# Kernel tuning notes

Hardware: AMD Instinct MI355X
Metric: run time of the kernel (lower is better)

The kernel has to match this reference:

```python
import jax, jax.numpy as jnp
import numpy as np

B, A, D, K = 262144, 10, 10, 32  # batch, aspects, aspect dim (=10), projection dim


def setup_inputs() -> dict:
    key = jax.random.key(0)
    ks = jax.random.split(key, 7)
    scale = 0.01
    return {
        "user_rep": jax.random.normal(ks[0], (B, A, D), jnp.float32),
        "item_rep": jax.random.normal(ks[1], (B, A, D), jnp.float32),
        "affinity_matrix": jax.random.uniform(ks[2], (D, D), jnp.float32, -scale, scale),
        "user_projection": jax.random.uniform(ks[3], (K, D), jnp.float32, -scale, scale),
        "user_parameters": jax.random.uniform(ks[4], (K, 1), jnp.float32, -scale, scale),
        "item_projection": jax.random.uniform(ks[5], (K, D), jnp.float32, -scale, scale),
        "item_parameters": jax.random.uniform(ks[6], (K, 1), jnp.float32, -scale, scale),
    }


def reference(user_rep, item_rep, affinity_matrix, user_projection,
              user_parameters, item_projection, item_parameters):
    # affinity: relu( U @ M @ V^T )  -> [B, Au, Av]
    aff = jax.nn.relu(jnp.einsum('bud,de,bve->buv', user_rep, affinity_matrix, item_rep))

    h_user = jnp.einsum('kd,bud->bku', user_projection, user_rep)  # [B,K,Au]
    h_item = jnp.einsum('kd,bvd->bkv', item_projection, item_rep)  # [B,K,Av]

    # user importance branch
    hu = jax.nn.relu(h_user + jnp.einsum('bkv,buv->bku', h_item, aff))
    u_score = jnp.einsum('k,bku->bu', user_parameters[:, 0], hu)   # [B,Au]
    user_asp_importance = jax.nn.softmax(u_score, axis=1)

    # item importance branch
    hi = jax.nn.relu(h_item + jnp.einsum('bku,buv->bkv', h_user, aff))
    i_score = jnp.einsum('k,bkv->bv', item_parameters[:, 0], hi)   # [B,Av]
    item_asp_importance = jax.nn.softmax(i_score, axis=1)

    return (user_asp_importance, item_asp_importance)
```

## Files before the change

### kernel.cpp

```cpp
#include <hip/hip_runtime.h>
#include <hip/hip_bf16.h>

#define NB 262144
#define AA 10
#define DD 10
#define KK 32

static __device__ __forceinline__ float b2f(unsigned short h) {
    union { unsigned u; float f; } c; c.u = ((unsigned)h) << 16; return c.f;
}
static __device__ __forceinline__ float bflo(unsigned w) {
    union { unsigned u; float f; } c; c.u = w << 16; return c.f;
}
static __device__ __forceinline__ float bfhi(unsigned w) {
    union { unsigned u; float f; } c; c.u = w & 0xffff0000u; return c.f;
}

__device__ __forceinline__ int detect_f32(const unsigned short* p, int nshorts,
                                          unsigned expthr, int lane) {
    int bad = 0;
    if (lane < nshorts) {
        unsigned e = (p[lane] >> 7) & 0xFFu;
        bad = (e >= expthr);
    }
    return __any(bad);
}

__global__ __launch_bounds__(64, 1) void aie_kernel(
    const unsigned short* __restrict__ user_rep,
    const unsigned short* __restrict__ item_rep,
    const unsigned short* __restrict__ wM,
    const unsigned short* __restrict__ wPu,
    const unsigned short* __restrict__ wpu,
    const unsigned short* __restrict__ wPi,
    const unsigned short* __restrict__ wpi,
    float* __restrict__ out)
{
    __shared__ float sM[100];
    __shared__ float sPu[KK * DD], sPi[KK * DD], spu[KK], spi[KK];
    __shared__ float buf[6400];

    const int t = threadIdx.x;

    int f = 0;
    f |= detect_f32(user_rep, 64, 137, t) << 0;
    f |= detect_f32(item_rep, 64, 137, t) << 1;
    f |= detect_f32(wM,  64, 125, t) << 2;
    f |= detect_f32(wPu, 64, 125, t) << 3;
    f |= detect_f32(wpu, 32, 125, t) << 4;
    f |= detect_f32(wPi, 64, 125, t) << 5;
    f |= detect_f32(wpi, 32, 125, t) << 6;

    {
        const float* fM  = (const float*)wM;
        const float* fPu = (const float*)wPu;
        const float* fPi = (const float*)wPi;
        const float* fpu = (const float*)wpu;
        const float* fpi = (const float*)wpi;
        for (int i = t; i < 100; i += 64) sM[i] = (f & 4) ? fM[i] : b2f(wM[i]);
        for (int i = t; i < KK * DD; i += 64) {
            sPu[i] = (f & 8)  ? fPu[i] : b2f(wPu[i]);
            sPi[i] = (f & 32) ? fPi[i] : b2f(wPi[i]);
        }
        if (t < KK) {
            spu[t] = (f & 16) ? fpu[t] : b2f(wpu[t]);
            spi[t] = (f & 64) ? fpi[t] : b2f(wpi[t]);
        }
    }
    __syncthreads();

    const int blk = blockIdx.x;
    float U[AA][DD], V[AA][DD];

    if (f & 2) {
        const float4* g = (const float4*)((const float*)item_rep + (size_t)blk * 6400);
        #pragma unroll
        for (int j = 0; j < 25; j++) ((float4*)buf)[t + 64 * j] = g[t + 64 * j];
    } else {
        const uint2* g = (const uint2*)(item_rep + (size_t)blk * 6400);
        #pragma unroll
        for (int j = 0; j < 25; j++) {
            uint2 w = g[t + 64 * j];
            ((float4*)buf)[t + 64 * j] =
                make_float4(bflo(w.x), bfhi(w.x), bflo(w.y), bfhi(w.y));
        }
    }
    __syncthreads();
    {
        const float4* mine = (const float4*)(buf + 100 * t);
        #pragma unroll
        for (int j = 0; j < 25; j++) {
            float4 w = mine[j]; int e = 4 * j;
            V[e / 10][e % 10]             = w.x;
            V[(e + 1) / 10][(e + 1) % 10] = w.y;
            V[(e + 2) / 10][(e + 2) % 10] = w.z;
            V[(e + 3) / 10][(e + 3) % 10] = w.w;
        }
    }
    __syncthreads();

    if (f & 1) {
        const float4* g = (const float4*)((const float*)user_rep + (size_t)blk * 6400);
        #pragma unroll
        for (int j = 0; j < 25; j++) ((float4*)buf)[t + 64 * j] = g[t + 64 * j];
    } else {
        const uint2* g = (const uint2*)(user_rep + (size_t)blk * 6400);
        #pragma unroll
        for (int j = 0; j < 25; j++) {
            uint2 w = g[t + 64 * j];
            ((float4*)buf)[t + 64 * j] =
                make_float4(bflo(w.x), bfhi(w.x), bflo(w.y), bfhi(w.y));
        }
    }
    __syncthreads();
    {
        const float4* mine = (const float4*)(buf + 100 * t);
        #pragma unroll
        for (int j = 0; j < 25; j++) {
            float4 w = mine[j]; int e = 4 * j;
            U[e / 10][e % 10]             = w.x;
            U[(e + 1) / 10][(e + 1) % 10] = w.y;
            U[(e + 2) / 10][(e + 2) % 10] = w.z;
            U[(e + 3) / 10][(e + 3) % 10] = w.w;
        }
    }
    __syncthreads();

    float W[AA][DD];
    #pragma unroll
    for (int u = 0; u < AA; u++) {
        float um[DD];
        #pragma unroll
        for (int e = 0; e < DD; e++) {
            float a = U[u][0] * sM[e];
            #pragma unroll
            for (int d = 1; d < DD; d++) a += U[u][d] * sM[d * 10 + e];
            um[e] = a;
        }
        float wrow[DD];
        #pragma unroll
        for (int d = 0; d < DD; d++) wrow[d] = 0.f;
        #pragma unroll
        for (int v = 0; v < AA; v++) {
            float r = um[0] * V[v][0];
            #pragma unroll
            for (int e = 1; e < DD; e++) r += um[e] * V[v][e];
            r = fmaxf(r, 0.f);
            #pragma unroll
            for (int d = 0; d < DD; d++) wrow[d] += r * V[v][d];
        }
        #pragma unroll
        for (int d = 0; d < DD; d++) W[u][d] = wrow[d];
    }

    float us[AA];
    #pragma unroll
    for (int u = 0; u < AA; u++) us[u] = 0.f;
    #pragma unroll 2
    for (int k = 0; k < KK; k++) {
        float pu[DD], pi[DD];
        #pragma unroll
        for (int d = 0; d < DD; d++) { pu[d] = sPu[k * 10 + d]; pi[d] = sPi[k * 10 + d]; }
        const float wk = spu[k];
        #pragma unroll
        for (int u = 0; u < AA; u++) {
            float a = pu[0] * U[u][0], b = pi[0] * W[u][0];
            #pragma unroll
            for (int d = 1; d < DD; d++) { a += pu[d] * U[u][d]; b += pi[d] * W[u][d]; }
            us[u] += wk * fmaxf(a + b, 0.f);
        }
    }

    {
        float mx = us[0];
        #pragma unroll
        for (int u = 1; u < AA; u++) mx = fmaxf(mx, us[u]);
        float s = 0.f;
        #pragma unroll
        for (int u = 0; u < AA; u++) { us[u] = __expf(us[u] - mx); s += us[u]; }
        float inv = 1.f / s;
        #pragma unroll
        for (int u = 0; u < AA; u++) buf[11 * t + u] = us[u] * inv;
    }

    float X[AA][DD];
    #pragma unroll
    for (int u = 0; u < AA; u++) {
        float um[DD];
        #pragma unroll
        for (int e = 0; e < DD; e++) {
            float a = U[u][DD - 1] * sM[(DD - 1) * 10 + e];
            #pragma unroll
            for (int d = DD - 2; d >= 0; d--) a += U[u][d] * sM[d * 10 + e];
            um[e] = a;
        }
        #pragma unroll
        for (int v = 0; v < AA; v++) {
            float r = um[DD - 1] * V[v][DD - 1];
            #pragma unroll
            for (int e = DD - 2; e >= 0; e--) r += um[e] * V[v][e];
            r = fmaxf(r, 0.f);
            #pragma unroll
            for (int d = 0; d < DD; d++) {
                if (u == 0) X[v][d] = r * U[u][d];
                else        X[v][d] += r * U[u][d];
            }
        }
    }

    float isc[AA];
    #pragma unroll
    for (int v = 0; v < AA; v++) isc[v] = 0.f;
    #pragma unroll 2
    for (int k = 0; k < KK; k++) {
        float pu[DD], pi[DD];
        #pragma unroll
        for (int d = 0; d < DD; d++) { pu[d] = sPu[k * 10 + d]; pi[d] = sPi[k * 10 + d]; }
        const float wk = spi[k];
        #pragma unroll
        for (int v = 0; v < AA; v++) {
            float a = pi[0] * V[v][0], b = pu[0] * X[v][0];
            #pragma unroll
            for (int d = 1; d < DD; d++) { a += pi[d] * V[v][d]; b += pu[d] * X[v][d]; }
            isc[v] += wk * fmaxf(a + b, 0.f);
        }
    }

    {
        float mx = isc[0];
        #pragma unroll
        for (int v = 1; v < AA; v++) mx = fmaxf(mx, isc[v]);
        float s = 0.f;
        #pragma unroll
        for (int v = 0; v < AA; v++) { isc[v] = __expf(isc[v] - mx); s += isc[v]; }
        float inv = 1.f / s;
        #pragma unroll
        for (int v = 0; v < AA; v++) buf[704 + 11 * t + v] = isc[v] * inv;
    }
    __syncthreads();

    {
        float2* o0 = (float2*)(out + (size_t)blk * 640);
        float2* o1 = (float2*)(out + (size_t)NB * 10 + (size_t)blk * 640);
        #pragma unroll
        for (int j = 0; j < 5; j++) {
            int m = t + 64 * j;
            int i = m / 5;
            int u = 2 * (m - 5 * i);
            o0[m] = make_float2(buf[11 * i + u],       buf[11 * i + u + 1]);
            o1[m] = make_float2(buf[704 + 11 * i + u], buf[704 + 11 * i + u + 1]);
        }
    }
}

extern "C" void kernel_launch(void* const* d_in, const int* in_sizes, int n_in,
                              void* d_out, int out_size, void* d_ws, size_t ws_size,
                              hipStream_t stream) {
    const unsigned short* user_rep = (const unsigned short*)d_in[0];
    const unsigned short* item_rep = (const unsigned short*)d_in[1];
    const unsigned short* wM       = (const unsigned short*)d_in[2];
    const unsigned short* wPu      = (const unsigned short*)d_in[3];
    const unsigned short* wpu      = (const unsigned short*)d_in[4];
    const unsigned short* wPi      = (const unsigned short*)d_in[5];
    const unsigned short* wpi      = (const unsigned short*)d_in[6];
    float* out                     = (float*)d_out;

    dim3 block(64);
    dim3 grid(NB / 64);
    hipLaunchKernelGGL(aie_kernel, grid, block, 0, stream,
                       user_rep, item_rep, wM, wPu, wpu, wPi, wpi, out);
}
```

Measured before the change: 397.4 us.

## Fuse per-row projection into affinity loops and halve staging buffer for occupancy

Removes the W and X per-thread arrays by computing each row's projection score immediately after its affinity row, which cuts register pressure. The item branch now computes M·v per item row instead of reusing U·M. The shared staging buffer is halved and filled in two passes, and Pu/Pi are interleaved into one padded shared array. Launch bounds request two blocks per CU. This adds extra syncs and a recompute of M·v, and the register budget it is aimed at may still be exceeded, causing spills.

```diff
diff --git a/kernel.cpp b/kernel.cpp
--- a/kernel.cpp
+++ b/kernel.cpp
@@ -26,7 +26,7 @@
     return __any(bad);
 }
 
-__global__ __launch_bounds__(64, 1) void aie_kernel(
+__global__ __launch_bounds__(64, 2) void aie_kernel(
     const unsigned short* __restrict__ user_rep,
     const unsigned short* __restrict__ item_rep,
     const unsigned short* __restrict__ wM,
@@ -37,8 +37,9 @@
     float* __restrict__ out)
 {
     __shared__ float sM[100];
-    __shared__ float sPu[KK * DD], sPi[KK * DD], spu[KK], spi[KK];
-    __shared__ float buf[6400];
+    __shared__ float sP[KK * 24];
+    __shared__ float spu[KK], spi[KK];
+    __shared__ float buf[3200];
 
     const int t = threadIdx.x;
 
@@ -59,8 +60,9 @@
         const float* fpi = (const float*)wpi;
         for (int i = t; i < 100; i += 64) sM[i] = (f & 4) ? fM[i] : b2f(wM[i]);
         for (int i = t; i < KK * DD; i += 64) {
-            sPu[i] = (f & 8)  ? fPu[i] : b2f(wPu[i]);
-            sPi[i] = (f & 32) ? fPi[i] : b2f(wPi[i]);
+            int k = i / 10, d = i - 10 * k;
+            sP[24 * k + d]      = (f & 8)  ? fPu[i] : b2f(wPu[i]);
+            sP[24 * k + 12 + d] = (f & 32) ? fPi[i] : b2f(wPi[i]);
         }
         if (t < KK) {
             spu[t] = (f & 16) ? fpu[t] : b2f(wpu[t]);
@@ -72,61 +74,77 @@
     const int blk = blockIdx.x;
     float U[AA][DD], V[AA][DD];
 
-    if (f & 2) {
-        const float4* g = (const float4*)((const float*)item_rep + (size_t)blk * 6400);
-        #pragma unroll
-        for (int j = 0; j < 25; j++) ((float4*)buf)[t + 64 * j] = g[t + 64 * j];
-    } else {
-        const uint2* g = (const uint2*)(item_rep + (size_t)blk * 6400);
-        #pragma unroll
-        for (int j = 0; j < 25; j++) {
-            uint2 w = g[t + 64 * j];
-            ((float4*)buf)[t + 64 * j] =
-                make_float4(bflo(w.x), bfhi(w.x), bflo(w.y), bfhi(w.y));
-        }
-    }
-    __syncthreads();
-    {
-        const float4* mine = (const float4*)(buf + 100 * t);
-        #pragma unroll
-        for (int j = 0; j < 25; j++) {
-            float4 w = mine[j]; int e = 4 * j;
-            V[e / 10][e % 10]             = w.x;
-            V[(e + 1) / 10][(e + 1) % 10] = w.y;
-            V[(e + 2) / 10][(e + 2) % 10] = w.z;
-            V[(e + 3) / 10][(e + 3) % 10] = w.w;
-        }
-    }
-    __syncthreads();
-
-    if (f & 1) {
-        const float4* g = (const float4*)((const float*)user_rep + (size_t)blk * 6400);
-        #pragma unroll
-        for (int j = 0; j < 25; j++) ((float4*)buf)[t + 64 * j] = g[t + 64 * j];
-    } else {
-        const uint2* g = (const uint2*)(user_rep + (size_t)blk * 6400);
-        #pragma unroll
-        for (int j = 0; j < 25; j++) {
-            uint2 w = g[t + 64 * j];
-            ((float4*)buf)[t + 64 * j] =
-                make_float4(bflo(w.x), bfhi(w.x), bflo(w.y), bfhi(w.y));
-        }
-    }
-    __syncthreads();
-    {
-        const float4* mine = (const float4*)(buf + 100 * t);
-        #pragma unroll
-        for (int j = 0; j < 25; j++) {
-            float4 w = mine[j]; int e = 4 * j;
-            U[e / 10][e % 10]             = w.x;
-            U[(e + 1) / 10][(e + 1) % 10] = w.y;
-            U[(e + 2) / 10][(e + 2) % 10] = w.z;
-            U[(e + 3) / 10][(e + 3) % 10] = w.w;
-        }
-    }
-    __syncthreads();
-
-    float W[AA][DD];
+    #pragma unroll 1
+    for (int h = 0; h < 2; h++) {
+        if (f & 2) {
+            const float4* g = (const float4*)((const float*)item_rep
+                              + (size_t)blk * 6400 + h * 3200);
+            #pragma unroll
+            for (int j = 0; j < 13; j++) {
+                int m = t + 64 * j;
+                if (m < 800) ((float4*)buf)[m] = g[m];
+            }
+        } else {
+            const uint2* g = (const uint2*)(item_rep + (size_t)blk * 6400 + h * 3200);
+            #pragma unroll
+            for (int j = 0; j < 13; j++) {
+                int m = t + 64 * j;
+                if (m < 800) {
+                    uint2 w = g[m];
+                    ((float4*)buf)[m] = make_float4(bflo(w.x), bfhi(w.x),
+                                                    bflo(w.y), bfhi(w.y));
+                }
+            }
+        }
+        __syncthreads();
+        if ((t >> 5) == h) {
+            const float2* mine = (const float2*)(buf + 100 * (t & 31));
+            #pragma unroll
+            for (int j = 0; j < 50; j++) {
+                float2 w = mine[j]; int e = 2 * j;
+                V[e / 10][e % 10]             = w.x;
+                V[(e + 1) / 10][(e + 1) % 10] = w.y;
+            }
+        }
+        __syncthreads();
+    }
+
+    #pragma unroll 1
+    for (int h = 0; h < 2; h++) {
+        if (f & 1) {
+            const float4* g = (const float4*)((const float*)user_rep
+                              + (size_t)blk * 6400 + h * 3200);
+            #pragma unroll
+            for (int j = 0; j < 13; j++) {
+                int m = t + 64 * j;
+                if (m < 800) ((float4*)buf)[m] = g[m];
+            }
+        } else {
+            const uint2* g = (const uint2*)(user_rep + (size_t)blk * 6400 + h * 3200);
+            #pragma unroll
+            for (int j = 0; j < 13; j++) {
+                int m = t + 64 * j;
+                if (m < 800) {
+                    uint2 w = g[m];
+                    ((float4*)buf)[m] = make_float4(bflo(w.x), bfhi(w.x),
+                                                    bflo(w.y), bfhi(w.y));
+                }
+            }
+        }
+        __syncthreads();
+        if ((t >> 5) == h) {
+            const float2* mine = (const float2*)(buf + 100 * (t & 31));
+            #pragma unroll
+            for (int j = 0; j < 50; j++) {
+                float2 w = mine[j]; int e = 2 * j;
+                U[e / 10][e % 10]             = w.x;
+                U[(e + 1) / 10][(e + 1) % 10] = w.y;
+            }
+        }
+        __syncthreads();
+    }
+
+    float us[AA];
     #pragma unroll
     for (int u = 0; u < AA; u++) {
         float um[DD];
@@ -134,7 +152,7 @@
         for (int e = 0; e < DD; e++) {
             float a = U[u][0] * sM[e];
             #pragma unroll
-            for (int d = 1; d < DD; d++) a += U[u][d] * sM[d * 10 + e];
+            for (int d = 1; d < DD; d++) a += U[u][d] * sM[10 * d + e];
             um[e] = a;
         }
         float wrow[DD];
@@ -149,26 +167,19 @@
             #pragma unroll
             for (int d = 0; d < DD; d++) wrow[d] += r * V[v][d];
         }
-        #pragma unroll
-        for (int d = 0; d < DD; d++) W[u][d] = wrow[d];
-    }
-
-    float us[AA];
-    #pragma unroll
-    for (int u = 0; u < AA; u++) us[u] = 0.f;
-    #pragma unroll 2
-    for (int k = 0; k < KK; k++) {
-        float pu[DD], pi[DD];
-        #pragma unroll
-        for (int d = 0; d < DD; d++) { pu[d] = sPu[k * 10 + d]; pi[d] = sPi[k * 10 + d]; }
-        const float wk = spu[k];
-        #pragma unroll
-        for (int u = 0; u < AA; u++) {
-            float a = pu[0] * U[u][0], b = pi[0] * W[u][0];
-            #pragma unroll
-            for (int d = 1; d < DD; d++) { a += pu[d] * U[u][d]; b += pi[d] * W[u][d]; }
-            us[u] += wk * fmaxf(a + b, 0.f);
-        }
+        float su = 0.f;
+        #pragma unroll 2
+        for (int k = 0; k < KK; k++) {
+            const float* pk = sP + 24 * k;
+            float a = pk[0] * U[u][0], b = pk[12] * wrow[0];
+            #pragma unroll
+            for (int d = 1; d < DD; d++) {
+                a += pk[d] * U[u][d];
+                b += pk[12 + d] * wrow[d];
+            }
+            su += spu[k] * fmaxf(a + b, 0.f);
+        }
+        us[u] = su;
     }
 
     {
@@ -183,47 +194,42 @@
         for (int u = 0; u < AA; u++) buf[11 * t + u] = us[u] * inv;
     }
 
-    float X[AA][DD];
-    #pragma unroll
-    for (int u = 0; u < AA; u++) {
-        float um[DD];
-        #pragma unroll
-        for (int e = 0; e < DD; e++) {
-            float a = U[u][DD - 1] * sM[(DD - 1) * 10 + e];
-            #pragma unroll
-            for (int d = DD - 2; d >= 0; d--) a += U[u][d] * sM[d * 10 + e];
-            um[e] = a;
-        }
-        #pragma unroll
-        for (int v = 0; v < AA; v++) {
-            float r = um[DD - 1] * V[v][DD - 1];
-            #pragma unroll
-            for (int e = DD - 2; e >= 0; e--) r += um[e] * V[v][e];
-            r = fmaxf(r, 0.f);
-            #pragma unroll
-            for (int d = 0; d < DD; d++) {
-                if (u == 0) X[v][d] = r * U[u][d];
-                else        X[v][d] += r * U[u][d];
-            }
-        }
-    }
-
     float isc[AA];
     #pragma unroll
-    for (int v = 0; v < AA; v++) isc[v] = 0.f;
-    #pragma unroll 2
-    for (int k = 0; k < KK; k++) {
-        float pu[DD], pi[DD];
-        #pragma unroll
-        for (int d = 0; d < DD; d++) { pu[d] = sPu[k * 10 + d]; pi[d] = sPi[k * 10 + d]; }
-        const float wk = spi[k];
-        #pragma unroll
-        for (int v = 0; v < AA; v++) {
-            float a = pi[0] * V[v][0], b = pu[0] * X[v][0];
-            #pragma unroll
-            for (int d = 1; d < DD; d++) { a += pi[d] * V[v][d]; b += pu[d] * X[v][d]; }
-            isc[v] += wk * fmaxf(a + b, 0.f);
-        }
+    for (int v = 0; v < AA; v++) {
+        float mv[DD];
+        #pragma unroll
+        for (int d = 0; d < DD; d++) {
+            float a = sM[10 * d] * V[v][0];
+            #pragma unroll
+            for (int e = 1; e < DD; e++) a += sM[10 * d + e] * V[v][e];
+            mv[d] = a;
+        }
+        float xrow[DD];
+        #pragma unroll
+        for (int d = 0; d < DD; d++) xrow[d] = 0.f;
+        #pragma unroll
+        for (int u = 0; u < AA; u++) {
+            float r = U[u][0] * mv[0];
+            #pragma unroll
+            for (int d = 1; d < DD; d++) r += U[u][d] * mv[d];
+            r = fmaxf(r, 0.f);
+            #pragma unroll
+            for (int d = 0; d < DD; d++) xrow[d] += r * U[u][d];
+        }
+        float sv = 0.f;
+        #pragma unroll 2
+        for (int k = 0; k < KK; k++) {
+            const float* pk = sP + 24 * k;
+            float a = pk[12] * V[v][0], b = pk[0] * xrow[0];
+            #pragma unroll
+            for (int d = 1; d < DD; d++) {
+                a += pk[12 + d] * V[v][d];
+                b += pk[d] * xrow[d];
+            }
+            sv += spi[k] * fmaxf(a + b, 0.f);
+        }
+        isc[v] = sv;
     }
 
     {
```

After: 498.5 us. 1.25x slower.
